# Kernel tuning notes

Hardware: AMD Instinct MI355X
Metric: run time of the kernel (lower is better)

## Reference

```python
import jax, jax.numpy as jnp
import numpy as np

B, T, C = 2, 2048, 2048
H, HKV = 32, 8
D = C // H            # head_dim = 64
G = H // HKV          # groups = 4
ROPE_BASE = 10000.0


def _rotate_half(x):
    x1, x2 = jnp.split(x, 2, axis=-1)
    return jnp.concatenate((-x2, x1), axis=-1)


def _rope_tables(seq_len, dim):
    inv_freq = 1.0 / (ROPE_BASE ** (jnp.arange(0, dim, 2, dtype=jnp.float32) / dim))
    t = jnp.arange(seq_len, dtype=jnp.float32)
    freqs = jnp.outer(t, inv_freq)          # [T, D/2]
    emb = jnp.concatenate((freqs, freqs), axis=-1)  # [T, D]
    return jnp.cos(emb), jnp.sin(emb)


def setup_inputs() -> dict:
    key = jax.random.key(0)
    ks = jax.random.split(key, 5)
    s = 0.02
    return {
        "x": jax.random.normal(ks[0], (B, T, C), jnp.float32),
        "Wq": jax.random.normal(ks[1], (C, C), jnp.float32) * s,
        "Wk": jax.random.normal(ks[2], (HKV * D, C), jnp.float32) * s,
        "Wv": jax.random.normal(ks[3], (HKV * D, C), jnp.float32) * s,
        "Wo": jax.random.normal(ks[4], (C, C), jnp.float32) * s,
    }


def reference(x, Wq, Wk, Wv, Wo):
    b, t, c = x.shape
    # fused QKV projections (nn.Linear: y = x @ W.T)
    q = (x @ Wq.T).reshape(b, t, H, D).transpose(0, 2, 1, 3)      # [B,H,T,D]
    k = (x @ Wk.T).reshape(b, t, HKV, D).transpose(0, 2, 1, 3)    # [B,HKV,T,D]
    v = (x @ Wv.T).reshape(b, t, HKV, D).transpose(0, 2, 1, 3)

    # RoPE (start_pos = 0)
    cos, sin = _rope_tables(t, D)           # [T, D] each
    cos = cos[None, None]                   # [1,1,T,D]
    sin = sin[None, None]
    q = q * cos + _rotate_half(q) * sin
    k = k * cos + _rotate_half(k) * sin

    # GQA head expansion (repeat_interleave on head dim)
    k = jnp.repeat(k, G, axis=1)            # [B,H,T,D]
    v = jnp.repeat(v, G, axis=1)

    # causal attention
    scale = 1.0 / jnp.sqrt(jnp.asarray(D, jnp.float32))
    scores = jnp.einsum('bhqd,bhkd->bhqk', q, k) * scale          # [B,H,T,T]
    causal = jnp.tril(jnp.ones((t, t), dtype=bool))
    scores = jnp.where(causal[None, None], scores, -jnp.inf)
    attn = jax.nn.softmax(scores.astype(jnp.float32), axis=-1).astype(q.dtype)
    out = jnp.einsum('bhqk,bhkd->bhqd', attn, v)                  # [B,H,T,D]
    out = out.transpose(0, 2, 1, 3).reshape(b, t, c)
    return out @ Wo.T
```

## Files before the change

kernel.cpp:

```cpp
#include <hip/hip_runtime.h>
#include <hip/hip_bf16.h>
#include <math.h>

typedef short short8 __attribute__((ext_vector_type(8)));
typedef float floatx4 __attribute__((ext_vector_type(4)));
typedef unsigned int uintx4 __attribute__((ext_vector_type(4)));
typedef int intx2 __attribute__((ext_vector_type(2)));

typedef __attribute__((address_space(1))) unsigned int as1_u32;
typedef __attribute__((address_space(3))) unsigned int as3_u32;

__device__ __forceinline__ void load_lds16(const void* g, void* l) {
  __builtin_amdgcn_global_load_lds((const as1_u32*)g, (as3_u32*)l, 16, 0, 0);
}

__device__ __forceinline__ unsigned short f2bf(float f) {
  __bf16 h = (__bf16)f;
  return __builtin_bit_cast(unsigned short, h);
}

__device__ __forceinline__ unsigned int pack_bf16(float a, float b) {
  return (unsigned int)f2bf(a) | ((unsigned int)f2bf(b) << 16);
}

#define MFMA16(a, b, c) __builtin_amdgcn_mfma_f32_16x16x32_bf16(a, b, c, 0, 0, 0)

#define TB 2
#define TT 2048
#define TC 2048
#define QKN 2560
#define KOFF 2048
#define SCALE_Q 0.18033688f

__global__ __launch_bounds__(256) void cast_all(
    const float* __restrict__ x, const float* __restrict__ wq,
    const float* __restrict__ wk, const float* __restrict__ wv,
    const float* __restrict__ wo,
    unsigned short* __restrict__ xb, unsigned short* __restrict__ wqkv,
    unsigned short* __restrict__ wob, float2* __restrict__ ropeTab) {
  if (blockIdx.x < 256) {
    const int idx = blockIdx.x * 256 + threadIdx.x;
    const int t = idx >> 5, d = idx & 31;
    const float inv = exp2f((float)d * -0.4152410119f);
    float sn, cs;
    sincosf((float)t * inv, &sn, &cs);
    ropeTab[idx] = make_float2(cs, sn);
  }
  long i4 = (long)blockIdx.x * 256 + threadIdx.x;
  const float* src;
  unsigned short* dst;
  if (i4 < 2097152)      { src = x;  dst = xb; }
  else if (i4 < 3145728) { src = wq; dst = wqkv;           i4 -= 2097152; }
  else if (i4 < 3407872) { src = wk; dst = wqkv + 4194304; i4 -= 3145728; }
  else if (i4 < 3670016) { src = wv; dst = wqkv + 5242880; i4 -= 3407872; }
  else                   { src = wo; dst = wob;            i4 -= 3670016; }
  float4 v = ((const float4*)src)[i4];
  ushort4 o;
  o.x = f2bf(v.x); o.y = f2bf(v.y); o.z = f2bf(v.z); o.w = f2bf(v.w);
  ((ushort4*)dst)[i4] = o;
}

__device__ __forceinline__ void gemm256_8ph(
    const unsigned short* __restrict__ A, const unsigned short* __restrict__ Bw,
    char* dynlds, int m0, int n0, int K, floatx4 (&acc)[8][4]) {
  const int tid = threadIdx.x;
  const int lane = tid & 63;
  const int w = tid >> 6;
  const int quad = lane >> 4, l15 = lane & 15;
  const int wm = w >> 2, wn = w & 3;

  const int srow8 = tid >> 3;
  const int schk = (tid & 7) ^ (srow8 & 7);
  const unsigned short* aS = A + (size_t)(m0 + srow8) * K + schk * 8;
  const unsigned short* bS = Bw + (size_t)(n0 + srow8) * K + schk * 8;

  const int key0 = (quad ^ (l15 & 7)) << 4;
  const int key1 = ((4 + quad) ^ (l15 & 7)) << 4;
  const int rdA = (wm * 16 + l15) * 128;
  const int rdB = 32768 + ((wn >> 1) * 64 + (wn & 1) * 16 + l15) * 128;

  const int NT = K >> 6;

  auto stage = [&](int bb, int isB, int h, int tt) {
    char* d = dynlds + bb * 65536 + isB * 32768 + h * 16384;
    const unsigned short* s = (isB ? bS : aS) + (size_t)tt * 64 + (size_t)(h * 128) * K;
    load_lds16(s, d + tid * 16);
    load_lds16(s + (size_t)64 * K, d + 8192 + tid * 16);
  };

  stage(0, 0, 0, 0); stage(0, 1, 0, 0); stage(0, 1, 1, 0); stage(0, 0, 1, 0);
  asm volatile("s_waitcnt vmcnt(4)" ::: "memory");
  __builtin_amdgcn_s_barrier();

  for (int t = 0; t < NT; ++t) {
    const int b = t & 1, nb = b ^ 1;
    const char* cb = dynlds + b * 65536;
    const bool STG = (t < NT - 1);
    short8 af[4][2], bfA[2][2], bfB[2][2];

#pragma unroll
    for (int i = 0; i < 4; ++i) {
      af[i][0] = *(const short8*)(cb + rdA + i * 4096 + key0);
      af[i][1] = *(const short8*)(cb + rdA + i * 4096 + key1);
    }
#pragma unroll
    for (int j = 0; j < 2; ++j) {
      bfA[j][0] = *(const short8*)(cb + rdB + j * 4096 + key0);
      bfA[j][1] = *(const short8*)(cb + rdB + j * 4096 + key1);
    }
    if (STG) {
      stage(nb, 0, 0, t + 1); stage(nb, 1, 0, t + 1);
      asm volatile("s_waitcnt vmcnt(4)" ::: "memory");
    } else {
      asm volatile("s_waitcnt vmcnt(0)" ::: "memory");
    }
    __builtin_amdgcn_s_barrier();
    asm volatile("s_waitcnt lgkmcnt(0)" ::: "memory");
    __builtin_amdgcn_s_setprio(1);
#pragma unroll
    for (int i = 0; i < 4; ++i)
#pragma unroll
      for (int j = 0; j < 2; ++j) {
        acc[i][j] = MFMA16(af[i][0], bfA[j][0], acc[i][j]);
        acc[i][j] = MFMA16(af[i][1], bfA[j][1], acc[i][j]);
      }
    __builtin_amdgcn_s_setprio(0);
    __builtin_amdgcn_s_barrier();

#pragma unroll
    for (int j = 0; j < 2; ++j) {
      bfB[j][0] = *(const short8*)(cb + rdB + 16384 + j * 4096 + key0);
      bfB[j][1] = *(const short8*)(cb + rdB + 16384 + j * 4096 + key1);
    }
    __builtin_amdgcn_s_barrier();
    asm volatile("s_waitcnt lgkmcnt(0)" ::: "memory");
    __builtin_amdgcn_s_setprio(1);
#pragma unroll
    for (int i = 0; i < 4; ++i)
#pragma unroll
      for (int j = 0; j < 2; ++j) {
        acc[i][j + 2] = MFMA16(af[i][0], bfB[j][0], acc[i][j + 2]);
        acc[i][j + 2] = MFMA16(af[i][1], bfB[j][1], acc[i][j + 2]);
      }
    __builtin_amdgcn_s_setprio(0);
    __builtin_amdgcn_s_barrier();

#pragma unroll
    for (int i = 0; i < 4; ++i) {
      af[i][0] = *(const short8*)(cb + rdA + (i + 4) * 4096 + key0);
      af[i][1] = *(const short8*)(cb + rdA + (i + 4) * 4096 + key1);
    }
    if (STG) { stage(nb, 1, 1, t + 1); stage(nb, 0, 1, t + 1); }
    __builtin_amdgcn_s_barrier();
    asm volatile("s_waitcnt lgkmcnt(0)" ::: "memory");
    __builtin_amdgcn_s_setprio(1);
#pragma unroll
    for (int i = 0; i < 4; ++i)
#pragma unroll
      for (int j = 0; j < 2; ++j) {
        acc[i + 4][j + 2] = MFMA16(af[i][0], bfB[j][0], acc[i + 4][j + 2]);
        acc[i + 4][j + 2] = MFMA16(af[i][1], bfB[j][1], acc[i + 4][j + 2]);
      }
    __builtin_amdgcn_s_setprio(0);
    __builtin_amdgcn_s_barrier();

    if (STG) asm volatile("s_waitcnt vmcnt(4)" ::: "memory");
    __builtin_amdgcn_s_barrier();
    __builtin_amdgcn_s_setprio(1);
#pragma unroll
    for (int i = 0; i < 4; ++i)
#pragma unroll
      for (int j = 0; j < 2; ++j) {
        acc[i + 4][j] = MFMA16(af[i][0], bfA[j][0], acc[i + 4][j]);
        acc[i + 4][j] = MFMA16(af[i][1], bfA[j][1], acc[i + 4][j]);
      }
    __builtin_amdgcn_s_setprio(0);
    __builtin_amdgcn_s_barrier();
  }
}

#define OUTCOL(n0, wn, j, l15) \
  ((n0) + ((j) >> 1) * 128 + ((wn) >> 1) * 64 + ((wn) & 1) * 16 + ((j) & 1) * 32 + (l15))

__global__ __launch_bounds__(512, 2) void gemm_qkv(const unsigned short* __restrict__ A,
                                                   const unsigned short* __restrict__ Bw,
                                                   unsigned short* __restrict__ qk,
                                                   unsigned short* __restrict__ vT,
                                                   const float2* __restrict__ ropeTab) {
  extern __shared__ char dynlds[];
  const int K = 2048;
  const int tid = threadIdx.x;
  const int lane = tid & 63, w = tid >> 6;
  const int quad = lane >> 4, l15 = lane & 15;
  const int wm = w >> 2, wn = w & 3;

  const int lin = blockIdx.y * 12 + blockIdx.x;
  const int wg = (lin & 7) * 24 + (lin >> 3);
  const int m0 = (wg / 12) * 256;
  const int n0 = (wg % 12) * 256;

  floatx4 acc[8][4];
#pragma unroll
  for (int i = 0; i < 8; ++i)
#pragma unroll
    for (int j = 0; j < 4; ++j) acc[i][j] = (floatx4){0.f, 0.f, 0.f, 0.f};

  gemm256_8ph(A, Bw, dynlds, m0, n0, K, acc);

  if (n0 < QKN) {
    const float qscale = (n0 < KOFF) ? SCALE_Q : 1.0f;
    const int d = (wn & 1) * 16 + l15;
#pragma unroll
    for (int i = 0; i < 8; ++i) {
      const int rowb = m0 + i * 32 + wm * 16 + quad * 4;
      const int tb = rowb & (TT - 1);
#pragma unroll
      for (int jp = 0; jp < 4; jp += 2) {
        const int col = OUTCOL(n0, wn, jp, l15);
#pragma unroll
        for (int r = 0; r < 4; ++r) {
          const float2 cssn = ropeTab[(tb + r) * 32 + d];
          const float a = acc[i][jp][r], b2 = acc[i][jp + 1][r];
          const float qa = (a * cssn.x - b2 * cssn.y) * qscale;
          const float qb = (b2 * cssn.x + a * cssn.y) * qscale;
          unsigned short* p = qk + (size_t)(rowb + r) * QKN + col;
          p[0] = f2bf(qa);
          p[32] = f2bf(qb);
        }
      }
    }
  } else {
#pragma unroll
    for (int i = 0; i < 8; ++i) {
      const int rowb = m0 + i * 32 + wm * 16 + quad * 4;
#pragma unroll
      for (int j = 0; j < 4; ++j) {
        const int col = OUTCOL(n0, wn, j, l15);
        ushort4 pk;
        pk.x = f2bf(acc[i][j][0]); pk.y = f2bf(acc[i][j][1]);
        pk.z = f2bf(acc[i][j][2]); pk.w = f2bf(acc[i][j][3]);
        *(ushort4*)(vT + (size_t)(col - 2560) * 4096 + rowb) = pk;
      }
    }
  }
}

__global__ __launch_bounds__(512, 2) void gemm_nt_f32(const unsigned short* __restrict__ A,
                                                      const unsigned short* __restrict__ Bw,
                                                      float* __restrict__ C,
                                                      int M, int N, int Kdim) {
  extern __shared__ char dynlds[];
  const int K = 2048;
  const int tid = threadIdx.x;
  const int lane = tid & 63, w = tid >> 6;
  const int quad = lane >> 4, l15 = lane & 15;
  const int wm = w >> 2, wn = w & 3;

  const int lin = blockIdx.y * 8 + blockIdx.x;
  const int wg = (lin & 7) * 16 + (lin >> 3);
  const int m0 = (wg >> 3) * 256;
  const int n0 = (wg & 7) * 256;

  floatx4 acc[8][4];
#pragma unroll
  for (int i = 0; i < 8; ++i)
#pragma unroll
    for (int j = 0; j < 4; ++j) acc[i][j] = (floatx4){0.f, 0.f, 0.f, 0.f};

  gemm256_8ph(A, Bw, dynlds, m0, n0, K, acc);

#pragma unroll
  for (int i = 0; i < 8; ++i) {
    const int row = m0 + i * 32 + wm * 16 + quad * 4;
#pragma unroll
    for (int j = 0; j < 4; ++j) {
      const int col = OUTCOL(n0, wn, j, l15);
#pragma unroll
      for (int r = 0; r < 4; ++r)
        C[(size_t)(row + r) * N + col] = acc[i][j][r];
    }
  }
}

__global__ __launch_bounds__(256, 3) void attn_kernel(const unsigned short* __restrict__ qk,
                                                      const unsigned short* __restrict__ vT,
                                                      unsigned short* __restrict__ attn) {
  const int h = blockIdx.x, b = blockIdx.y;
  const int qt = 15 - (int)blockIdx.z;
  const int hk = h >> 2;
  const int tid = threadIdx.x;
  const int w = tid >> 6, lane = tid & 63, quad = lane >> 4, l15 = lane & 15;

  __shared__ char lds[32768];

  const int srow = tid >> 3;
  const int sgrp = ((tid & 7) ^ (srow & 7));
  const int relbase = w * 32 + l15;

  const short8 ones = {16256, 16256, 16256, 16256, 16256, 16256, 16256, 16256};

  const size_t rowQ = (size_t)(b * TT + qt * 128);

  {
    const unsigned short* qsrc = qk + (rowQ + srow) * QKN + h * 64 + sgrp * 8;
#pragma unroll
    for (int p = 0; p < 4; ++p)
      load_lds16(qsrc + (size_t)p * 32 * QKN, lds + p * 4096 + tid * 16);
  }
  __syncthreads();
  short8 qf[2][2];
#pragma unroll
  for (int i = 0; i < 2; ++i)
#pragma unroll
    for (int ks = 0; ks < 2; ++ks)
      qf[i][ks] = *(const short8*)(lds + (w * 32 + i * 16 + l15) * 128 +
                                   ((((ks << 2) + quad) ^ (l15 & 7)) << 4));
  __syncthreads();

  floatx4 accO[2][4], accL[2];
#pragma unroll
  for (int i = 0; i < 2; ++i) {
    accL[i] = (floatx4){0.f, 0.f, 0.f, 0.f};
#pragma unroll
    for (int j = 0; j < 4; ++j) accO[i][j] = (floatx4){0.f, 0.f, 0.f, 0.f};
  }

  const unsigned short* kptr =
      qk + (size_t)(b * TT + srow) * QKN + KOFF + hk * 64 + sgrp * 8;
  const unsigned short* vptr =
      vT + (size_t)(hk * 64 + srow) * 4096 + b * TT + sgrp * 8;

  load_lds16(kptr, lds + tid * 16);
  load_lds16(kptr + (size_t)32 * QKN, lds + 4096 + tid * 16);
  load_lds16(vptr, lds + 16384 + tid * 16);
  load_lds16(vptr + (size_t)32 * 4096, lds + 16384 + 4096 + tid * 16);
  kptr += (size_t)64 * QKN;
  vptr += 64;
  __syncthreads();

  auto step = [&](const int BUF, const bool PREF, const int MREL) {
    if (PREF) {
      char* kd = lds + ((BUF ^ 1) * 8192);
      char* vd = lds + 16384 + ((BUF ^ 1) * 8192);
      load_lds16(kptr, kd + tid * 16);
      load_lds16(kptr + (size_t)32 * QKN, kd + 4096 + tid * 16);
      load_lds16(vptr, vd + tid * 16);
      load_lds16(vptr + (size_t)32 * 4096, vd + 4096 + tid * 16);
      kptr += (size_t)64 * QKN;
      vptr += 64;
    }

    const char* Ks = lds + BUF * 8192;
    floatx4 st[2][4];
    __builtin_amdgcn_s_setprio(1);
#pragma unroll
    for (int jm = 0; jm < 4; ++jm) {
      const int krow = jm * 16 + l15;
      const short8 kf0 = *(const short8*)(Ks + krow * 128 + ((quad ^ (l15 & 7)) << 4));
      const short8 kf1 = *(const short8*)(Ks + krow * 128 + (((4 + quad) ^ (l15 & 7)) << 4));
#pragma unroll
      for (int i = 0; i < 2; ++i) {
        floatx4 z = (floatx4){0.f, 0.f, 0.f, 0.f};
        z = __builtin_amdgcn_mfma_f32_16x16x32_bf16(kf0, qf[i][0], z, 0, 0, 0);
        st[i][jm] = __builtin_amdgcn_mfma_f32_16x16x32_bf16(kf1, qf[i][1], z, 0, 0, 0);
      }
    }
    __builtin_amdgcn_s_setprio(0);

    const char* Vt = lds + 16384 + BUF * 8192;
    short8 vf[2][4];
#pragma unroll
    for (int ks = 0; ks < 2; ++ks)
#pragma unroll
      for (int jd = 0; jd < 4; ++jd) {
        const int d = jd * 16 + l15;
        vf[ks][jd] = *(const short8*)(Vt + d * 128 +
                                      ((((ks << 2) + quad) ^ (l15 & 7)) << 4));
      }

    short8 pT[2][2];
#pragma unroll
    for (int i = 0; i < 2; ++i) {
      unsigned int U[4][2];
#pragma unroll
      for (int jm = 0; jm < 4; ++jm) {
        float e0 = __builtin_amdgcn_exp2f(st[i][jm][0]);
        float e1 = __builtin_amdgcn_exp2f(st[i][jm][1]);
        float e2 = __builtin_amdgcn_exp2f(st[i][jm][2]);
        float e3 = __builtin_amdgcn_exp2f(st[i][jm][3]);
        if (MREL >= 0) {
          const int rel = relbase + i * 16 - MREL;
          const int kg = jm * 16 + quad * 4;
          if (kg > rel) e0 = 0.f;
          if (kg + 1 > rel) e1 = 0.f;
          if (kg + 2 > rel) e2 = 0.f;
          if (kg + 3 > rel) e3 = 0.f;
        }
        U[jm][0] = pack_bf16(e0, e1);
        U[jm][1] = pack_bf16(e2, e3);
      }
#pragma unroll
      for (int ks = 0; ks < 2; ++ks) {
        uintx4 t;
#pragma unroll
        for (int hh = 0; hh < 2; ++hh) {
          intx2 r32 = __builtin_amdgcn_permlane32_swap(
              (int)U[2 * ks][hh], (int)U[2 * ks + 1][hh], false, false);
          intx2 r16 = __builtin_amdgcn_permlane16_swap(r32[0], r32[1], false, false);
          t[hh] = (unsigned int)r16[0];
          t[2 + hh] = (unsigned int)r16[1];
        }
        pT[i][ks] = __builtin_bit_cast(short8, t);
      }
    }

    __builtin_amdgcn_s_setprio(1);
#pragma unroll
    for (int ks = 0; ks < 2; ++ks) {
      accL[0] = __builtin_amdgcn_mfma_f32_16x16x32_bf16(pT[0][ks], ones, accL[0], 0, 0, 0);
      accL[1] = __builtin_amdgcn_mfma_f32_16x16x32_bf16(pT[1][ks], ones, accL[1], 0, 0, 0);
#pragma unroll
      for (int jd = 0; jd < 4; ++jd) {
        accO[0][jd] = __builtin_amdgcn_mfma_f32_16x16x32_bf16(pT[0][ks], vf[ks][jd], accO[0][jd], 0, 0, 0);
        accO[1][jd] = __builtin_amdgcn_mfma_f32_16x16x32_bf16(pT[1][ks], vf[ks][jd], accO[1][jd], 0, 0, 0);
      }
    }
    __builtin_amdgcn_s_setprio(0);
    __syncthreads();
  };

  for (int t2 = 0; t2 < qt; ++t2) {
    step(0, true, -1);
    step(1, true, -1);
  }
  step(0, true, 0);
  step(1, false, 64);

#pragma unroll
  for (int i2 = 0; i2 < 2; ++i2) {
    floatx4 rl;
#pragma unroll
    for (int r = 0; r < 4; ++r) rl[r] = __builtin_amdgcn_rcpf(accL[i2][r]);
#pragma unroll
    for (int jd = 0; jd < 4; ++jd) {
      const int col = h * 64 + jd * 16 + l15;
#pragma unroll
      for (int r = 0; r < 4; ++r) {
        const size_t row = rowQ + w * 32 + i2 * 16 + quad * 4 + r;
        attn[row * TC + col] = f2bf(accO[i2][jd][r] * rl[r]);
      }
    }
  }
}

extern "C" void kernel_launch(void* const* d_in, const int* in_sizes, int n_in,
                              void* d_out, int out_size, void* d_ws, size_t ws_size,
                              hipStream_t stream) {
  const float* x = (const float*)d_in[0];
  const float* Wq = (const float*)d_in[1];
  const float* Wk = (const float*)d_in[2];
  const float* Wv = (const float*)d_in[3];
  const float* Wo = (const float*)d_in[4];
  float* out = (float*)d_out;

  char* ws = (char*)d_ws;
  unsigned short* xb   = (unsigned short*)(ws);
  unsigned short* wqkv = (unsigned short*)(ws + 16777216);
  unsigned short* wob  = (unsigned short*)(ws + 29360128);
  unsigned short* qk   = (unsigned short*)(ws + 37748736);
  unsigned short* vT   = (unsigned short*)(ws + 58720256);
  unsigned short* attn = (unsigned short*)(ws + 62914560);
  float2* ropeTab = (float2*)(ws + 62914560);

  cast_all<<<18432, 256, 0, stream>>>(x, Wq, Wk, Wv, Wo, xb, wqkv, wob, ropeTab);
  gemm_qkv<<<dim3(12, 16), 512, 131072, stream>>>(xb, wqkv, qk, vT, ropeTab);
  attn_kernel<<<dim3(32, 2, 16), 256, 0, stream>>>(qk, vT, attn);
  gemm_nt_f32<<<dim3(8, 16), 512, 131072, stream>>>(attn, wob, out, 4096, TC, 2048);
}
```

Before: 268.0 us.

## Restructure 256x256 GEMM mainloop into two-tile unrolled pipeline with finer-grained staging

The bf16 GEMM mainloop is unrolled by two K-tiles with fixed LDS buffers. Global-to-LDS loads for the next tiles are now issued one quarter-tile at a time, as soon as each quarter of the buffer has been consumed, so data arrives earlier and is spread across the MFMA phases. One barrier before the last MFMA phase is dropped. This aims to hide global-load latency better, at the cost of a more delicate waitcnt/barrier schedule that risks races if the vmcnt accounting is off.

```diff
diff --git a/kernel.cpp b/kernel.cpp
--- a/kernel.cpp
+++ b/kernel.cpp
@@ -60,6 +60,18 @@
   ((ushort4*)dst)[i4] = o;
 }
 
+#define MFMA_QUAD(I0, J0, BF)                                                  \
+  __builtin_amdgcn_s_setprio(1);                                               \
+  _Pragma("unroll") for (int i_ = 0; i_ < 4; ++i_) {                           \
+    _Pragma("unroll") for (int j_ = 0; j_ < 2; ++j_) {                         \
+      acc[(I0) + i_][(J0) + j_] =                                              \
+          MFMA16(af[i_][0], BF[j_][0], acc[(I0) + i_][(J0) + j_]);             \
+      acc[(I0) + i_][(J0) + j_] =                                              \
+          MFMA16(af[i_][1], BF[j_][1], acc[(I0) + i_][(J0) + j_]);             \
+    }                                                                          \
+  }                                                                            \
+  __builtin_amdgcn_s_setprio(0);
+
 __device__ __forceinline__ void gemm256_8ph(
     const unsigned short* __restrict__ A, const unsigned short* __restrict__ Bw,
     char* dynlds, int m0, int n0, int K, floatx4 (&acc)[8][4]) {
@@ -79,7 +91,7 @@
   const int rdA = (wm * 16 + l15) * 128;
   const int rdB = 32768 + ((wn >> 1) * 64 + (wn & 1) * 16 + l15) * 128;
 
-  const int NT = K >> 6;
+  const int NIT = K >> 7;
 
   auto stage = [&](int bb, int isB, int h, int tt) {
     char* d = dynlds + bb * 65536 + isB * 32768 + h * 16384;
@@ -89,92 +101,104 @@
   };
 
   stage(0, 0, 0, 0); stage(0, 1, 0, 0); stage(0, 1, 1, 0); stage(0, 0, 1, 0);
+  stage(1, 0, 0, 1); stage(1, 1, 1, 1);
   asm volatile("s_waitcnt vmcnt(4)" ::: "memory");
   __builtin_amdgcn_s_barrier();
 
-  for (int t = 0; t < NT; ++t) {
-    const int b = t & 1, nb = b ^ 1;
-    const char* cb = dynlds + b * 65536;
-    const bool STG = (t < NT - 1);
-    short8 af[4][2], bfA[2][2], bfB[2][2];
+  short8 af[4][2], bfA[2][2], bfB[2][2];
+  const char* cb0 = dynlds;
+  const char* cb1 = dynlds + 65536;
+
+  for (int it = 0; it < NIT; ++it) {
+    const int tO = it * 2 + 1, tE2 = it * 2 + 2, tO2 = it * 2 + 3;
+    const bool STG = (it < NIT - 1);
 
 #pragma unroll
     for (int i = 0; i < 4; ++i) {
-      af[i][0] = *(const short8*)(cb + rdA + i * 4096 + key0);
-      af[i][1] = *(const short8*)(cb + rdA + i * 4096 + key1);
+      af[i][0] = *(const short8*)(cb0 + rdA + i * 4096 + key0);
+      af[i][1] = *(const short8*)(cb0 + rdA + i * 4096 + key1);
     }
 #pragma unroll
     for (int j = 0; j < 2; ++j) {
-      bfA[j][0] = *(const short8*)(cb + rdB + j * 4096 + key0);
-      bfA[j][1] = *(const short8*)(cb + rdB + j * 4096 + key1);
-    }
-    if (STG) {
-      stage(nb, 0, 0, t + 1); stage(nb, 1, 0, t + 1);
-      asm volatile("s_waitcnt vmcnt(4)" ::: "memory");
-    } else {
-      asm volatile("s_waitcnt vmcnt(0)" ::: "memory");
-    }
+      bfA[j][0] = *(const short8*)(cb0 + rdB + j * 4096 + key0);
+      bfA[j][1] = *(const short8*)(cb0 + rdB + j * 4096 + key1);
+    }
+    stage(1, 1, 0, tO);
     __builtin_amdgcn_s_barrier();
     asm volatile("s_waitcnt lgkmcnt(0)" ::: "memory");
-    __builtin_amdgcn_s_setprio(1);
-#pragma unroll
-    for (int i = 0; i < 4; ++i)
-#pragma unroll
-      for (int j = 0; j < 2; ++j) {
-        acc[i][j] = MFMA16(af[i][0], bfA[j][0], acc[i][j]);
-        acc[i][j] = MFMA16(af[i][1], bfA[j][1], acc[i][j]);
-      }
-    __builtin_amdgcn_s_setprio(0);
+    MFMA_QUAD(0, 0, bfA)
     __builtin_amdgcn_s_barrier();
 
 #pragma unroll
     for (int j = 0; j < 2; ++j) {
-      bfB[j][0] = *(const short8*)(cb + rdB + 16384 + j * 4096 + key0);
-      bfB[j][1] = *(const short8*)(cb + rdB + 16384 + j * 4096 + key1);
-    }
+      bfB[j][0] = *(const short8*)(cb0 + rdB + 16384 + j * 4096 + key0);
+      bfB[j][1] = *(const short8*)(cb0 + rdB + 16384 + j * 4096 + key1);
+    }
+    stage(1, 0, 1, tO);
     __builtin_amdgcn_s_barrier();
     asm volatile("s_waitcnt lgkmcnt(0)" ::: "memory");
-    __builtin_amdgcn_s_setprio(1);
-#pragma unroll
-    for (int i = 0; i < 4; ++i)
-#pragma unroll
-      for (int j = 0; j < 2; ++j) {
-        acc[i][j + 2] = MFMA16(af[i][0], bfB[j][0], acc[i][j + 2]);
-        acc[i][j + 2] = MFMA16(af[i][1], bfB[j][1], acc[i][j + 2]);
-      }
-    __builtin_amdgcn_s_setprio(0);
+    MFMA_QUAD(0, 2, bfB)
     __builtin_amdgcn_s_barrier();
 
 #pragma unroll
     for (int i = 0; i < 4; ++i) {
-      af[i][0] = *(const short8*)(cb + rdA + (i + 4) * 4096 + key0);
-      af[i][1] = *(const short8*)(cb + rdA + (i + 4) * 4096 + key1);
-    }
-    if (STG) { stage(nb, 1, 1, t + 1); stage(nb, 0, 1, t + 1); }
+      af[i][0] = *(const short8*)(cb0 + rdA + (i + 4) * 4096 + key0);
+      af[i][1] = *(const short8*)(cb0 + rdA + (i + 4) * 4096 + key1);
+    }
+    if (STG) stage(0, 0, 0, tE2);
     __builtin_amdgcn_s_barrier();
     asm volatile("s_waitcnt lgkmcnt(0)" ::: "memory");
-    __builtin_amdgcn_s_setprio(1);
-#pragma unroll
-    for (int i = 0; i < 4; ++i)
-#pragma unroll
-      for (int j = 0; j < 2; ++j) {
-        acc[i + 4][j + 2] = MFMA16(af[i][0], bfB[j][0], acc[i + 4][j + 2]);
-        acc[i + 4][j + 2] = MFMA16(af[i][1], bfB[j][1], acc[i + 4][j + 2]);
-      }
-    __builtin_amdgcn_s_setprio(0);
-    __builtin_amdgcn_s_barrier();
-
+    MFMA_QUAD(4, 2, bfB)
+    __builtin_amdgcn_s_barrier();
+
+    if (STG) stage(0, 1, 1, tE2);
+    MFMA_QUAD(4, 0, bfA)
     if (STG) asm volatile("s_waitcnt vmcnt(4)" ::: "memory");
-    __builtin_amdgcn_s_barrier();
-    __builtin_amdgcn_s_setprio(1);
-#pragma unroll
-    for (int i = 0; i < 4; ++i)
-#pragma unroll
-      for (int j = 0; j < 2; ++j) {
-        acc[i + 4][j] = MFMA16(af[i][0], bfA[j][0], acc[i + 4][j]);
-        acc[i + 4][j] = MFMA16(af[i][1], bfA[j][1], acc[i + 4][j]);
-      }
-    __builtin_amdgcn_s_setprio(0);
+    else     asm volatile("s_waitcnt vmcnt(0)" ::: "memory");
+    __builtin_amdgcn_s_barrier();
+
+#pragma unroll
+    for (int i = 0; i < 4; ++i) {
+      af[i][0] = *(const short8*)(cb1 + rdA + i * 4096 + key0);
+      af[i][1] = *(const short8*)(cb1 + rdA + i * 4096 + key1);
+    }
+#pragma unroll
+    for (int j = 0; j < 2; ++j) {
+      bfA[j][0] = *(const short8*)(cb1 + rdB + j * 4096 + key0);
+      bfA[j][1] = *(const short8*)(cb1 + rdB + j * 4096 + key1);
+    }
+    if (STG) stage(0, 1, 0, tE2);
+    __builtin_amdgcn_s_barrier();
+    asm volatile("s_waitcnt lgkmcnt(0)" ::: "memory");
+    MFMA_QUAD(0, 0, bfA)
+    __builtin_amdgcn_s_barrier();
+
+#pragma unroll
+    for (int j = 0; j < 2; ++j) {
+      bfB[j][0] = *(const short8*)(cb1 + rdB + 16384 + j * 4096 + key0);
+      bfB[j][1] = *(const short8*)(cb1 + rdB + 16384 + j * 4096 + key1);
+    }
+    if (STG) stage(0, 0, 1, tE2);
+    __builtin_amdgcn_s_barrier();
+    asm volatile("s_waitcnt lgkmcnt(0)" ::: "memory");
+    MFMA_QUAD(0, 2, bfB)
+    __builtin_amdgcn_s_barrier();
+
+#pragma unroll
+    for (int i = 0; i < 4; ++i) {
+      af[i][0] = *(const short8*)(cb1 + rdA + (i + 4) * 4096 + key0);
+      af[i][1] = *(const short8*)(cb1 + rdA + (i + 4) * 4096 + key1);
+    }
+    if (STG) stage(1, 0, 0, tO2);
+    __builtin_amdgcn_s_barrier();
+    asm volatile("s_waitcnt lgkmcnt(0)" ::: "memory");
+    MFMA_QUAD(4, 2, bfB)
+    __builtin_amdgcn_s_barrier();
+
+    if (STG) stage(1, 1, 1, tO2);
+    MFMA_QUAD(4, 0, bfA)
+    if (STG) asm volatile("s_waitcnt vmcnt(4)" ::: "memory");
+    else     asm volatile("s_waitcnt vmcnt(0)" ::: "memory");
     __builtin_amdgcn_s_barrier();
   }
 }
```

Measured after the change: 263.9 us. No clear change (-1.5%).
